# Optimization experiments

Hardware: AMD Instinct MI355X
Metric: run time of the kernel (lower is better)

The kernel has to match this reference:

```python
import jax, jax.numpy as jnp
import numpy as np

N_STEPS = 3000
DT = 0.02


def make_phi_t(n=N_STEPS, dt=DT):
    # Central-difference first-derivative operator with one-sided 2nd-order ends.
    P = np.zeros((n, n), dtype=np.float32)
    P[0, 0:3] = [-1.5, 2.0, -0.5]
    idx = np.arange(1, n - 1)
    P[idx, idx - 1] = -0.5
    P[idx, idx + 1] = 0.5
    P[n - 1, n - 3:] = [0.5, -2.0, 1.5]
    return jnp.asarray(P / dt)


def lstm_layer(x, w_ih, w_hh, b_ih, b_hh):
    # x: [B, T, I]; PyTorch gate order i, f, g, o along the 4H axis.
    B, T, _ = x.shape
    H = w_hh.shape[1]
    x_proj = jnp.einsum('bti,gi->btg', x, w_ih) + b_ih + b_hh  # [B, T, 4H]

    def step(carry, xt):
        h, c = carry
        gates = xt + h @ w_hh.T  # [B, 4H]
        i, f, g, o = jnp.split(gates, 4, axis=-1)
        c = jax.nn.sigmoid(f) * c + jax.nn.sigmoid(i) * jnp.tanh(g)
        h = jax.nn.sigmoid(o) * jnp.tanh(c)
        return (h, c), h

    h0 = jnp.zeros((B, H), x.dtype)
    (_, _), hs = jax.lax.scan(step, (h0, h0), x_proj.transpose(1, 0, 2))
    return hs.transpose(1, 0, 2)  # [B, T, H]


def setup_inputs() -> dict:
    key = jax.random.key(0)
    B, T, I, H = 64, N_STEPS, 8, 128
    ks = jax.random.split(key, 16)
    s = lambda k, shape, fan: (jax.random.normal(k, shape, jnp.float32) / np.sqrt(fan)).astype(jnp.float32)
    return {
        'x': jax.random.normal(ks[0], (B, T, I), jnp.float32),
        'w_ih0': s(ks[1], (4 * H, I), I), 'w_hh0': s(ks[2], (4 * H, H), H),
        'b_ih0': s(ks[3], (4 * H,), H), 'b_hh0': s(ks[4], (4 * H,), H),
        'w_ih1': s(ks[5], (4 * H, H), H), 'w_hh1': s(ks[6], (4 * H, H), H),
        'b_ih1': s(ks[7], (4 * H,), H), 'b_hh1': s(ks[8], (4 * H,), H),
        'fc1_w': s(ks[9], (16, H), H), 'fc1_b': s(ks[10], (16,), H),
        'fc2_w': s(ks[11], (4, 16), 16), 'fc2_b': s(ks[12], (4,), 16),
        'fc3_w': s(ks[13], (1, 4), 4), 'fc3_b': s(ks[14], (1,), 4),
    }


def reference(x, w_ih0, w_hh0, b_ih0, b_hh0, w_ih1, w_hh1, b_ih1, b_hh1,
              fc1_w, fc1_b, fc2_w, fc2_b, fc3_w, fc3_b):
    phi = make_phi_t()  # fixed [3000, 3000] FD operator (buffer, not learned)
    h = lstm_layer(x, w_ih0, w_hh0, b_ih0, b_hh0)
    h = lstm_layer(h, w_ih1, w_hh1, b_ih1, b_hh1)
    h = jax.nn.relu(h @ fc1_w.T + fc1_b)
    h = jax.nn.relu(h @ fc2_w.T + fc2_b)
    y = h @ fc3_w.T + fc3_b            # [B, T, 1]
    yt = y[:, :, 0].T                  # [T, B]
    x_tt = phi @ (phi @ yt)            # double derivative via dense matmuls
    return x_tt.T[:, :, None]          # [B, T, 1]
```

## Files before the change

kernel.cpp:

```cpp
#include <hip/hip_runtime.h>
#include <math.h>


#define T_STEPS 3000
#define BATCH   64
#define HID     128
#define CHUNK   10
#define INV_DT  50.0f

__device__ __forceinline__ float sigmoid_(float x) {
    return 1.0f / (1.0f + __expf(-x));
}
__device__ __forceinline__ float tanh_(float x) {
    return 1.0f - 2.0f / (__expf(2.0f * x) + 1.0f);
}

__global__ void __launch_bounds__(512)
lstm_layer0(const float* __restrict__ x,
            const float* __restrict__ w_ih,
            const float* __restrict__ w_hh,
            const float* __restrict__ b_ih,
            const float* __restrict__ b_hh,
            float* __restrict__ h_out)
{
    const int b   = blockIdx.x;
    const int tid = threadIdx.x;
    const int j   = tid >> 2;
    const int gt  = tid & 3;
    const int r   = gt * HID + j;
    const int rot = (tid & 7) << 2;

    __shared__ __align__(16) float Wl[512 * 64];
    __shared__ __align__(16) float h_s[2][HID];

    float w[64];
#pragma unroll
    for (int i = 0; i < 64; i += 4) {
        float4 v = *(const float4*)(w_hh + (size_t)r * HID + i);
        w[i] = v.x; w[i+1] = v.y; w[i+2] = v.z; w[i+3] = v.w;
    }
#pragma unroll
    for (int i = 0; i < 64; i += 4) {
        float4 v = *(const float4*)(w_hh + (size_t)r * HID + 64 + i);
        *(float4*)&Wl[tid * 64 + (i ^ rot)] = v;
    }
    float wi[8];
#pragma unroll
    for (int i = 0; i < 8; i += 4) {
        float4 v = *(const float4*)(w_ih + (size_t)r * 8 + i);
        wi[i] = v.x; wi[i+1] = v.y; wi[i+2] = v.z; wi[i+3] = v.w;
    }
    const float bias = b_ih[r] + b_hh[r];
    float c = 0.0f;

    if (tid < HID) h_s[0][tid] = 0.0f;
    __syncthreads();

    const float* xrow = x + (size_t)b * T_STEPS * 8;
    float* hb = h_out + (size_t)b * T_STEPS * HID;

#pragma unroll 1
    for (int t = 0; t < T_STEPS; ++t) {
        const int rb = t & 1;
        float4 xa = *(const float4*)(xrow + t * 8);
        float4 xc = *(const float4*)(xrow + t * 8 + 4);
        float a0 = bias
                 + wi[0]*xa.x + wi[1]*xa.y + wi[2]*xa.z + wi[3]*xa.w
                 + wi[4]*xc.x + wi[5]*xc.y + wi[6]*xc.z + wi[7]*xc.w;
        float a1 = 0.f, a2 = 0.f, a3 = 0.f;
        float b0 = 0.f, b1 = 0.f, b2 = 0.f, b3 = 0.f;

#pragma unroll
        for (int k4 = 0; k4 < 16; k4 += 4) {
            float4 h0 = *(const float4*)(&h_s[rb][4*k4]);
            float4 h1 = *(const float4*)(&h_s[rb][4*k4 + 4]);
            float4 h2 = *(const float4*)(&h_s[rb][4*k4 + 8]);
            float4 h3 = *(const float4*)(&h_s[rb][4*k4 + 12]);
            a0 += w[4*k4   ]*h0.x + w[4*k4+ 1]*h0.y + w[4*k4+ 2]*h0.z + w[4*k4+ 3]*h0.w;
            a1 += w[4*k4+ 4]*h1.x + w[4*k4+ 5]*h1.y + w[4*k4+ 6]*h1.z + w[4*k4+ 7]*h1.w;
            a2 += w[4*k4+ 8]*h2.x + w[4*k4+ 9]*h2.y + w[4*k4+10]*h2.z + w[4*k4+11]*h2.w;
            a3 += w[4*k4+12]*h3.x + w[4*k4+13]*h3.y + w[4*k4+14]*h3.z + w[4*k4+15]*h3.w;
        }
        {
            const float* wlp = &Wl[tid * 64];
#pragma unroll
            for (int i = 0; i < 64; i += 16) {
                float4 g0 = *(const float4*)(wlp + ((i     ) ^ rot));
                float4 g1 = *(const float4*)(wlp + ((i +  4) ^ rot));
                float4 g2 = *(const float4*)(wlp + ((i +  8) ^ rot));
                float4 g3 = *(const float4*)(wlp + ((i + 12) ^ rot));
                float4 h0 = *(const float4*)(&h_s[rb][64 + i]);
                float4 h1 = *(const float4*)(&h_s[rb][64 + i + 4]);
                float4 h2 = *(const float4*)(&h_s[rb][64 + i + 8]);
                float4 h3 = *(const float4*)(&h_s[rb][64 + i + 12]);
                b0 += g0.x*h0.x + g0.y*h0.y + g0.z*h0.z + g0.w*h0.w;
                b1 += g1.x*h1.x + g1.y*h1.y + g1.z*h1.z + g1.w*h1.w;
                b2 += g2.x*h2.x + g2.y*h2.y + g2.z*h2.z + g2.w*h2.w;
                b3 += g3.x*h3.x + g3.y*h3.y + g3.z*h3.z + g3.w*h3.w;
            }
        }
        float acc = ((a0 + a1) + (a2 + a3)) + ((b0 + b1) + (b2 + b3));

        float av = (gt == 2) ? tanh_(acc) : sigmoid_(acc);
        float t1 = __shfl_xor(av, 1);
        float t2 = __shfl_xor(av, 2);
        float t3 = __shfl_xor(t1, 2);
        if (gt == 0) {
            c = t1 * c + av * t2;
            float h = t3 * tanh_(c);
            h_s[rb ^ 1][j] = h;
            hb[(size_t)t * HID + j] = h;
        }
        __syncthreads();
    }
}

__global__ void __launch_bounds__(512)
lstm_layer1(const float* __restrict__ w_ih,
            const float* __restrict__ w_hh,
            const float* __restrict__ b_ih,
            const float* __restrict__ b_hh,
            float* __restrict__ h_buf)
{
    const int b   = blockIdx.x;
    const int tid = threadIdx.x;
    const int j   = tid >> 2;
    const int gt  = tid & 3;
    const int r   = gt * HID + j;
    const int rot = (tid & 7) << 2;

    __shared__ __align__(16) float Wl[512 * 64];
    __shared__ __align__(16) float h_s[2][HID];

    float w[64];
#pragma unroll
    for (int i = 0; i < 64; i += 4) {
        float4 v = *(const float4*)(w_hh + (size_t)r * HID + i);
        w[i] = v.x; w[i+1] = v.y; w[i+2] = v.z; w[i+3] = v.w;
    }
#pragma unroll
    for (int i = 0; i < 64; i += 4) {
        float4 v = *(const float4*)(w_hh + (size_t)r * HID + 64 + i);
        *(float4*)&Wl[tid * 64 + (i ^ rot)] = v;
    }
    const float bias = b_ih[r] + b_hh[r];
    float c = 0.0f;
    if (tid < HID) h_s[0][tid] = 0.0f;
    __syncthreads();

    float* hbB = h_buf + (size_t)b * T_STEPS * HID;
    const float* wihr = w_ih + (size_t)r * HID;

    for (int t0 = 0; t0 < T_STEPS; t0 += CHUNK) {
        float acc[CHUNK];
#pragma unroll
        for (int tau = 0; tau < CHUNK; ++tau) acc[tau] = bias;
        const float* hp = hbB + (size_t)t0 * HID;
#pragma unroll 2
        for (int k4 = 0; k4 < 32; ++k4) {
            float4 w4 = *(const float4*)(wihr + 4 * k4);
#pragma unroll
            for (int tau = 0; tau < CHUNK; ++tau) {
                float4 h4 = *(const float4*)(hp + tau * HID + 4 * k4);
                acc[tau] += w4.x*h4.x + w4.y*h4.y + w4.z*h4.z + w4.w*h4.w;
            }
        }
        __syncthreads();

#pragma unroll
        for (int tt = 0; tt < CHUNK; ++tt) {
            const int rb = tt & 1;
            float a0 = acc[tt];
            float a1 = 0.f, a2 = 0.f, a3 = 0.f;
            float b0 = 0.f, b1 = 0.f, b2 = 0.f, b3 = 0.f;
#pragma unroll
            for (int k4 = 0; k4 < 16; k4 += 4) {
                float4 h0 = *(const float4*)(&h_s[rb][4*k4]);
                float4 h1 = *(const float4*)(&h_s[rb][4*k4 + 4]);
                float4 h2 = *(const float4*)(&h_s[rb][4*k4 + 8]);
                float4 h3 = *(const float4*)(&h_s[rb][4*k4 + 12]);
                a0 += w[4*k4   ]*h0.x + w[4*k4+ 1]*h0.y + w[4*k4+ 2]*h0.z + w[4*k4+ 3]*h0.w;
                a1 += w[4*k4+ 4]*h1.x + w[4*k4+ 5]*h1.y + w[4*k4+ 6]*h1.z + w[4*k4+ 7]*h1.w;
                a2 += w[4*k4+ 8]*h2.x + w[4*k4+ 9]*h2.y + w[4*k4+10]*h2.z + w[4*k4+11]*h2.w;
                a3 += w[4*k4+12]*h3.x + w[4*k4+13]*h3.y + w[4*k4+14]*h3.z + w[4*k4+15]*h3.w;
            }
            {
                const float* wlp = &Wl[tid * 64];
#pragma unroll
                for (int i = 0; i < 64; i += 16) {
                    float4 g0 = *(const float4*)(wlp + ((i     ) ^ rot));
                    float4 g1 = *(const float4*)(wlp + ((i +  4) ^ rot));
                    float4 g2 = *(const float4*)(wlp + ((i +  8) ^ rot));
                    float4 g3 = *(const float4*)(wlp + ((i + 12) ^ rot));
                    float4 h0 = *(const float4*)(&h_s[rb][64 + i]);
                    float4 h1 = *(const float4*)(&h_s[rb][64 + i + 4]);
                    float4 h2 = *(const float4*)(&h_s[rb][64 + i + 8]);
                    float4 h3 = *(const float4*)(&h_s[rb][64 + i + 12]);
                    b0 += g0.x*h0.x + g0.y*h0.y + g0.z*h0.z + g0.w*h0.w;
                    b1 += g1.x*h1.x + g1.y*h1.y + g1.z*h1.z + g1.w*h1.w;
                    b2 += g2.x*h2.x + g2.y*h2.y + g2.z*h2.z + g2.w*h2.w;
                    b3 += g3.x*h3.x + g3.y*h3.y + g3.z*h3.z + g3.w*h3.w;
                }
            }
            float acs = ((a0 + a1) + (a2 + a3)) + ((b0 + b1) + (b2 + b3));

            float av = (gt == 2) ? tanh_(acs) : sigmoid_(acs);
            float t1 = __shfl_xor(av, 1);
            float t2 = __shfl_xor(av, 2);
            float t3 = __shfl_xor(t1, 2);
            if (gt == 0) {
                c = t1 * c + av * t2;
                float h = t3 * tanh_(c);
                h_s[rb ^ 1][j] = h;
                hbB[(size_t)(t0 + tt) * HID + j] = h;
            }
            __syncthreads();
        }
    }
}

__global__ void __launch_bounds__(256)
fc_head(const float* __restrict__ h_buf,
        const float* __restrict__ fc1_w, const float* __restrict__ fc1_b,
        const float* __restrict__ fc2_w, const float* __restrict__ fc2_b,
        const float* __restrict__ fc3_w, const float* __restrict__ fc3_b,
        float* __restrict__ y_bt)
{
    __shared__ __align__(16) float w1[16 * HID];
    __shared__ float sb[89];
    const int tid = threadIdx.x;
    for (int i = tid; i < 16 * HID; i += 256) w1[i] = fc1_w[i];
    if (tid < 16) sb[tid]      = fc1_b[tid];
    if (tid < 64) sb[16 + tid] = fc2_w[tid];
    if (tid < 4)  sb[80 + tid] = fc2_b[tid];
    if (tid < 4)  sb[84 + tid] = fc3_w[tid];
    if (tid == 0) sb[88]       = fc3_b[0];
    __syncthreads();

    const int idx = blockIdx.x * 256 + tid;
    if (idx >= BATCH * T_STEPS) return;
    const float* h = h_buf + (size_t)idx * HID;

    float y1[16];
#pragma unroll
    for (int jo = 0; jo < 16; ++jo) y1[jo] = sb[jo];
#pragma unroll 4
    for (int k4 = 0; k4 < 32; ++k4) {
        float4 hv = *(const float4*)(h + 4 * k4);
#pragma unroll
        for (int jo = 0; jo < 16; ++jo) {
            float4 wv = *(const float4*)(&w1[jo * HID + 4 * k4]);
            y1[jo] += wv.x*hv.x + wv.y*hv.y + wv.z*hv.z + wv.w*hv.w;
        }
    }
    float y2[4];
#pragma unroll
    for (int jo = 0; jo < 4; ++jo) {
        float a = sb[80 + jo];
#pragma unroll
        for (int k = 0; k < 16; ++k) a += sb[16 + jo * 16 + k] * fmaxf(y1[k], 0.0f);
        y2[jo] = fmaxf(a, 0.0f);
    }
    float y = sb[88];
#pragma unroll
    for (int k = 0; k < 4; ++k) y += sb[84 + k] * y2[k];

    y_bt[idx] = y;
}

__global__ void deriv_k(const float* __restrict__ in,
                        float* __restrict__ outp)
{
    const int idx = blockIdx.x * blockDim.x + threadIdx.x;
    if (idx >= BATCH * T_STEPS) return;
    const int t = idx % T_STEPS;
    float v;
    if (t == 0) {
        v = (-1.5f * in[idx] + 2.0f * in[idx + 1] - 0.5f * in[idx + 2]) * INV_DT;
    } else if (t == T_STEPS - 1) {
        v = (0.5f * in[idx - 2] - 2.0f * in[idx - 1] + 1.5f * in[idx]) * INV_DT;
    } else {
        v = (in[idx + 1] - in[idx - 1]) * (0.5f * INV_DT);
    }
    outp[idx] = v;
}

extern "C" void kernel_launch(void* const* d_in, const int* in_sizes, int n_in,
                              void* d_out, int out_size, void* d_ws, size_t ws_size,
                              hipStream_t stream)
{
    const float* x     = (const float*)d_in[0];
    const float* w_ih0 = (const float*)d_in[1];
    const float* w_hh0 = (const float*)d_in[2];
    const float* b_ih0 = (const float*)d_in[3];
    const float* b_hh0 = (const float*)d_in[4];
    const float* w_ih1 = (const float*)d_in[5];
    const float* w_hh1 = (const float*)d_in[6];
    const float* b_ih1 = (const float*)d_in[7];
    const float* b_hh1 = (const float*)d_in[8];
    const float* fc1_w = (const float*)d_in[9];
    const float* fc1_b = (const float*)d_in[10];
    const float* fc2_w = (const float*)d_in[11];
    const float* fc2_b = (const float*)d_in[12];
    const float* fc3_w = (const float*)d_in[13];
    const float* fc3_b = (const float*)d_in[14];
    float* out = (float*)d_out;

    float* h_buf = (float*)d_ws;
    float* y_bt  = (float*)((char*)d_ws + 98304000);
    float* z_bt  = (float*)((char*)d_ws + 98304000 + 768000);

    lstm_layer0<<<dim3(BATCH), dim3(512), 0, stream>>>(x, w_ih0, w_hh0, b_ih0, b_hh0, h_buf);
    lstm_layer1<<<dim3(BATCH), dim3(512), 0, stream>>>(w_ih1, w_hh1, b_ih1, b_hh1, h_buf);

    const int nelem = T_STEPS * BATCH;
    fc_head<<<dim3(nelem / 256), dim3(256), 0, stream>>>(
        h_buf, fc1_w, fc1_b, fc2_w, fc2_b, fc3_w, fc3_b, y_bt);
    deriv_k<<<dim3(nelem / 256), dim3(256), 0, stream>>>(y_bt, z_bt);
    deriv_k<<<dim3(nelem / 256), dim3(256), 0, stream>>>(z_bt, out);
}
```

Baseline: 15.69 ms.

## Split-K LSTM recurrence across thread quads and precompute layer-1 input projection

Each hidden unit's four-thread group now splits the K dimension, with each thread computing all four gates over a quarter of the hidden state and combining them through cross-lane shuffles. The h vector is padded in shared memory to avoid bank conflicts. For layer 1, a new parallel kernel computes the input projection for all timesteps into a large workspace buffer, so the sequential recurrence only reads one precomputed value per step, prefetched one step ahead. This takes serial matmul work off the critical path but costs about 393 MB of extra global traffic, and it falls back to the fused kernel when the workspace is too small.

```diff
diff --git a/kernel.cpp b/kernel.cpp
--- a/kernel.cpp
+++ b/kernel.cpp
@@ -5,7 +5,6 @@
 #define T_STEPS 3000
 #define BATCH   64
 #define HID     128
-#define CHUNK   10
 #define INV_DT  50.0f
 
 __device__ __forceinline__ float sigmoid_(float x) {
@@ -26,34 +25,35 @@
     const int b   = blockIdx.x;
     const int tid = threadIdx.x;
     const int j   = tid >> 2;
-    const int gt  = tid & 3;
-    const int r   = gt * HID + j;
-    const int rot = (tid & 7) << 2;
-
-    __shared__ __align__(16) float Wl[512 * 64];
-    __shared__ __align__(16) float h_s[2][HID];
-
-    float w[64];
-#pragma unroll
-    for (int i = 0; i < 64; i += 4) {
-        float4 v = *(const float4*)(w_hh + (size_t)r * HID + i);
-        w[i] = v.x; w[i+1] = v.y; w[i+2] = v.z; w[i+3] = v.w;
-    }
-#pragma unroll
-    for (int i = 0; i < 64; i += 4) {
-        float4 v = *(const float4*)(w_hh + (size_t)r * HID + 64 + i);
-        *(float4*)&Wl[tid * 64 + (i ^ rot)] = v;
-    }
+    const int q   = tid & 3;
+    const int kq  = q * 32;
+
+    __shared__ __align__(16) float4 Wl4[8 * 512];
+    __shared__ __align__(16) float  h_pad[2][160];
+
+    float w[96];
+#pragma unroll
+    for (int g = 0; g < 3; ++g) {
+#pragma unroll
+        for (int i = 0; i < 32; i += 4) {
+            float4 v = *(const float4*)(w_hh + (size_t)(g * HID + j) * HID + kq + i);
+            w[g*32 + i] = v.x; w[g*32 + i+1] = v.y; w[g*32 + i+2] = v.z; w[g*32 + i+3] = v.w;
+        }
+    }
+#pragma unroll
+    for (int i = 0; i < 8; ++i)
+        Wl4[i * 512 + tid] = *(const float4*)(w_hh + (size_t)(3 * HID + j) * HID + kq + 4 * i);
+
     float wi[8];
 #pragma unroll
     for (int i = 0; i < 8; i += 4) {
-        float4 v = *(const float4*)(w_ih + (size_t)r * 8 + i);
+        float4 v = *(const float4*)(w_ih + (size_t)(q * HID + j) * 8 + i);
         wi[i] = v.x; wi[i+1] = v.y; wi[i+2] = v.z; wi[i+3] = v.w;
     }
-    const float bias = b_ih[r] + b_hh[r];
+    const float bias = b_ih[q * HID + j] + b_hh[q * HID + j];
     float c = 0.0f;
 
-    if (tid < HID) h_s[0][tid] = 0.0f;
+    if (tid < 160) h_pad[0][tid] = 0.0f;
     __syncthreads();
 
     const float* xrow = x + (size_t)b * T_STEPS * 8;
@@ -64,51 +64,36 @@
         const int rb = t & 1;
         float4 xa = *(const float4*)(xrow + t * 8);
         float4 xc = *(const float4*)(xrow + t * 8 + 4);
-        float a0 = bias
-                 + wi[0]*xa.x + wi[1]*xa.y + wi[2]*xa.z + wi[3]*xa.w
-                 + wi[4]*xc.x + wi[5]*xc.y + wi[6]*xc.z + wi[7]*xc.w;
-        float a1 = 0.f, a2 = 0.f, a3 = 0.f;
-        float b0 = 0.f, b1 = 0.f, b2 = 0.f, b3 = 0.f;
-
-#pragma unroll
-        for (int k4 = 0; k4 < 16; k4 += 4) {
-            float4 h0 = *(const float4*)(&h_s[rb][4*k4]);
-            float4 h1 = *(const float4*)(&h_s[rb][4*k4 + 4]);
-            float4 h2 = *(const float4*)(&h_s[rb][4*k4 + 8]);
-            float4 h3 = *(const float4*)(&h_s[rb][4*k4 + 12]);
-            a0 += w[4*k4   ]*h0.x + w[4*k4+ 1]*h0.y + w[4*k4+ 2]*h0.z + w[4*k4+ 3]*h0.w;
-            a1 += w[4*k4+ 4]*h1.x + w[4*k4+ 5]*h1.y + w[4*k4+ 6]*h1.z + w[4*k4+ 7]*h1.w;
-            a2 += w[4*k4+ 8]*h2.x + w[4*k4+ 9]*h2.y + w[4*k4+10]*h2.z + w[4*k4+11]*h2.w;
-            a3 += w[4*k4+12]*h3.x + w[4*k4+13]*h3.y + w[4*k4+14]*h3.z + w[4*k4+15]*h3.w;
-        }
-        {
-            const float* wlp = &Wl[tid * 64];
-#pragma unroll
-            for (int i = 0; i < 64; i += 16) {
-                float4 g0 = *(const float4*)(wlp + ((i     ) ^ rot));
-                float4 g1 = *(const float4*)(wlp + ((i +  4) ^ rot));
-                float4 g2 = *(const float4*)(wlp + ((i +  8) ^ rot));
-                float4 g3 = *(const float4*)(wlp + ((i + 12) ^ rot));
-                float4 h0 = *(const float4*)(&h_s[rb][64 + i]);
-                float4 h1 = *(const float4*)(&h_s[rb][64 + i + 4]);
-                float4 h2 = *(const float4*)(&h_s[rb][64 + i + 8]);
-                float4 h3 = *(const float4*)(&h_s[rb][64 + i + 12]);
-                b0 += g0.x*h0.x + g0.y*h0.y + g0.z*h0.z + g0.w*h0.w;
-                b1 += g1.x*h1.x + g1.y*h1.y + g1.z*h1.z + g1.w*h1.w;
-                b2 += g2.x*h2.x + g2.y*h2.y + g2.z*h2.z + g2.w*h2.w;
-                b3 += g3.x*h3.x + g3.y*h3.y + g3.z*h3.z + g3.w*h3.w;
-            }
-        }
-        float acc = ((a0 + a1) + (a2 + a3)) + ((b0 + b1) + (b2 + b3));
-
-        float av = (gt == 2) ? tanh_(acc) : sigmoid_(acc);
+        float xterm = bias
+                    + wi[0]*xa.x + wi[1]*xa.y + wi[2]*xa.z + wi[3]*xa.w
+                    + wi[4]*xc.x + wi[5]*xc.y + wi[6]*xc.z + wi[7]*xc.w;
+
+        float a0 = 0.f, a1 = 0.f, a2 = 0.f, a3 = 0.f;
+        const float* hq = &h_pad[rb][40 * q];
+#pragma unroll
+        for (int i = 0; i < 8; ++i) {
+            float4 hv = *(const float4*)(hq + 4 * i);
+            float4 g4 = Wl4[i * 512 + tid];
+            a0 += w[     4*i]*hv.x + w[     4*i+1]*hv.y + w[     4*i+2]*hv.z + w[     4*i+3]*hv.w;
+            a1 += w[32 + 4*i]*hv.x + w[32 + 4*i+1]*hv.y + w[32 + 4*i+2]*hv.z + w[32 + 4*i+3]*hv.w;
+            a2 += w[64 + 4*i]*hv.x + w[64 + 4*i+1]*hv.y + w[64 + 4*i+2]*hv.z + w[64 + 4*i+3]*hv.w;
+            a3 += g4.x*hv.x + g4.y*hv.y + g4.z*hv.z + g4.w*hv.w;
+        }
+        float s0 = __shfl_xor((q & 1) ? a0 : a1, 1);
+        float s1 = __shfl_xor((q & 1) ? a2 : a3, 1);
+        float p0 = ((q & 1) ? a1 : a0) + s0;
+        float p1 = ((q & 1) ? a3 : a2) + s1;
+        float S  = ((q & 2) ? p1 : p0) + __shfl_xor((q & 2) ? p0 : p1, 2);
+        S += xterm;
+
+        float av = (q == 2) ? tanh_(S) : sigmoid_(S);
         float t1 = __shfl_xor(av, 1);
         float t2 = __shfl_xor(av, 2);
         float t3 = __shfl_xor(t1, 2);
-        if (gt == 0) {
+        if (q == 0) {
             c = t1 * c + av * t2;
             float h = t3 * tanh_(c);
-            h_s[rb ^ 1][j] = h;
+            h_pad[rb ^ 1][(j & 31) + 40 * (j >> 5)] = h;
             hb[(size_t)t * HID + j] = h;
         }
         __syncthreads();
@@ -116,11 +101,119 @@
 }
 
 __global__ void __launch_bounds__(512)
-lstm_layer1(const float* __restrict__ w_ih,
-            const float* __restrict__ w_hh,
-            const float* __restrict__ b_ih,
-            const float* __restrict__ b_hh,
-            float* __restrict__ h_buf)
+xp_proj(const float* __restrict__ w_ih,
+        const float* __restrict__ b_ih,
+        const float* __restrict__ b_hh,
+        const float* __restrict__ h1,
+        float* __restrict__ xp)
+{
+    const int blk = blockIdx.x;
+    const int b   = blk / 125;
+    const int t0  = (blk % 125) * 24;
+    const int r   = threadIdx.x;
+
+    float acc[24];
+    const float bias = b_ih[r] + b_hh[r];
+#pragma unroll
+    for (int u = 0; u < 24; ++u) acc[u] = bias;
+
+    const float* hp = h1 + ((size_t)b * T_STEPS + t0) * HID;
+    const float* wr = w_ih + (size_t)r * HID;
+#pragma unroll 2
+    for (int k4 = 0; k4 < 32; ++k4) {
+        float4 w4 = *(const float4*)(wr + 4 * k4);
+#pragma unroll
+        for (int u = 0; u < 24; ++u) {
+            float4 h4 = *(const float4*)(hp + u * HID + 4 * k4);
+            acc[u] += w4.x*h4.x + w4.y*h4.y + w4.z*h4.z + w4.w*h4.w;
+        }
+    }
+    float* xo = xp + ((size_t)b * T_STEPS + t0) * 512 + r;
+#pragma unroll
+    for (int u = 0; u < 24; ++u) xo[(size_t)u * 512] = acc[u];
+}
+
+__global__ void __launch_bounds__(512)
+lstm_layer1_pre(const float* __restrict__ w_hh,
+                const float* __restrict__ xp,
+                float* __restrict__ h_buf)
+{
+    const int b   = blockIdx.x;
+    const int tid = threadIdx.x;
+    const int j   = tid >> 2;
+    const int q   = tid & 3;
+    const int kq  = q * 32;
+
+    __shared__ __align__(16) float4 Wl4[8 * 512];
+    __shared__ __align__(16) float  h_pad[2][160];
+
+    float w[96];
+#pragma unroll
+    for (int g = 0; g < 3; ++g) {
+#pragma unroll
+        for (int i = 0; i < 32; i += 4) {
+            float4 v = *(const float4*)(w_hh + (size_t)(g * HID + j) * HID + kq + i);
+            w[g*32 + i] = v.x; w[g*32 + i+1] = v.y; w[g*32 + i+2] = v.z; w[g*32 + i+3] = v.w;
+        }
+    }
+#pragma unroll
+    for (int i = 0; i < 8; ++i)
+        Wl4[i * 512 + tid] = *(const float4*)(w_hh + (size_t)(3 * HID + j) * HID + kq + 4 * i);
+
+    float c = 0.0f;
+    if (tid < 160) h_pad[0][tid] = 0.0f;
+    __syncthreads();
+
+    float* hb = h_buf + (size_t)b * T_STEPS * HID;
+    const float* xpb = xp + (size_t)b * T_STEPS * 512 + q * HID + j;
+
+    float xq = xpb[0];
+#pragma unroll 1
+    for (int t = 0; t < T_STEPS; ++t) {
+        const int rb = t & 1;
+        const int tn = (t + 1 < T_STEPS) ? t + 1 : t;
+        float xq_n = xpb[(size_t)tn * 512];
+
+        float a0 = 0.f, a1 = 0.f, a2 = 0.f, a3 = 0.f;
+        const float* hq = &h_pad[rb][40 * q];
+#pragma unroll
+        for (int i = 0; i < 8; ++i) {
+            float4 hv = *(const float4*)(hq + 4 * i);
+            float4 g4 = Wl4[i * 512 + tid];
+            a0 += w[     4*i]*hv.x + w[     4*i+1]*hv.y + w[     4*i+2]*hv.z + w[     4*i+3]*hv.w;
+            a1 += w[32 + 4*i]*hv.x + w[32 + 4*i+1]*hv.y + w[32 + 4*i+2]*hv.z + w[32 + 4*i+3]*hv.w;
+            a2 += w[64 + 4*i]*hv.x + w[64 + 4*i+1]*hv.y + w[64 + 4*i+2]*hv.z + w[64 + 4*i+3]*hv.w;
+            a3 += g4.x*hv.x + g4.y*hv.y + g4.z*hv.z + g4.w*hv.w;
+        }
+        float s0 = __shfl_xor((q & 1) ? a0 : a1, 1);
+        float s1 = __shfl_xor((q & 1) ? a2 : a3, 1);
+        float p0 = ((q & 1) ? a1 : a0) + s0;
+        float p1 = ((q & 1) ? a3 : a2) + s1;
+        float S  = ((q & 2) ? p1 : p0) + __shfl_xor((q & 2) ? p0 : p1, 2);
+        S += xq;
+
+        float av = (q == 2) ? tanh_(S) : sigmoid_(S);
+        float t1 = __shfl_xor(av, 1);
+        float t2 = __shfl_xor(av, 2);
+        float t3 = __shfl_xor(t1, 2);
+        if (q == 0) {
+            c = t1 * c + av * t2;
+            float h = t3 * tanh_(c);
+            h_pad[rb ^ 1][(j & 31) + 40 * (j >> 5)] = h;
+            hb[(size_t)t * HID + j] = h;
+        }
+        xq = xq_n;
+        __syncthreads();
+    }
+}
+
+#define CHUNK   10
+__global__ void __launch_bounds__(512)
+lstm_layer1_fused(const float* __restrict__ w_ih,
+                  const float* __restrict__ w_hh,
+                  const float* __restrict__ b_ih,
+                  const float* __restrict__ b_hh,
+                  float* __restrict__ h_buf)
 {
     const int b   = blockIdx.x;
     const int tid = threadIdx.x;
@@ -309,9 +402,17 @@
     float* h_buf = (float*)d_ws;
     float* y_bt  = (float*)((char*)d_ws + 98304000);
     float* z_bt  = (float*)((char*)d_ws + 98304000 + 768000);
+    float* xp    = (float*)((char*)d_ws + 98304000 + 1536000);
+    const bool use_pre = ws_size >= (size_t)98304000 + 1536000 + 393216000;
 
     lstm_layer0<<<dim3(BATCH), dim3(512), 0, stream>>>(x, w_ih0, w_hh0, b_ih0, b_hh0, h_buf);
-    lstm_layer1<<<dim3(BATCH), dim3(512), 0, stream>>>(w_ih1, w_hh1, b_ih1, b_hh1, h_buf);
+
+    if (use_pre) {
+        xp_proj<<<dim3(BATCH * 125), dim3(512), 0, stream>>>(w_ih1, b_ih1, b_hh1, h_buf, xp);
+        lstm_layer1_pre<<<dim3(BATCH), dim3(512), 0, stream>>>(w_hh1, xp, h_buf);
+    } else {
+        lstm_layer1_fused<<<dim3(BATCH), dim3(512), 0, stream>>>(w_ih1, w_hh1, b_ih1, b_hh1, h_buf);
+    }
 
     const int nelem = T_STEPS * BATCH;
     fc_head<<<dim3(nelem / 256), dim3(256), 0, stream>>>(
```

Result: faster. 14.08 ms (-10.2%).
